# Performance work log

Measured on AMD Instinct MI355X. Metric: run time of the kernel, lower is better.

The kernel has to match this reference:

```python
import jax, jax.numpy as jnp
import numpy as np


def setup_inputs() -> dict:
    key = jax.random.key(0)
    k1, k2 = jax.random.split(key)
    pred = jax.random.normal(k1, (4, 8192, 3), dtype=jnp.float32)
    target = jax.random.normal(k2, (4, 8192, 3), dtype=jnp.float32)
    return {"pred": pred, "target": target}


def reference(pred, target):
    # Pairwise squared distances via the expansion ||p-q||^2 = ||p||^2 + ||q||^2 - 2 p.q
    # Avoids materializing the O(B*M*N*3) diff tensor of the naive broadcast.
    p_sq = jnp.sum(pred * pred, axis=-1)          # [B, M]
    q_sq = jnp.sum(target * target, axis=-1)      # [B, N]
    cross = jnp.einsum("bmd,bnd->bmn", pred, target)  # [B, M, N]
    dist_sq = p_sq[:, :, None] + q_sq[:, None, :] - 2.0 * cross  # [B, M, N]
    min_dist_pred = jnp.min(dist_sq, axis=2).mean(axis=1)    # [B] min over target per pred point
    min_dist_target = jnp.min(dist_sq, axis=1).mean(axis=1)  # [B] min over pred per target point
    return jnp.mean(min_dist_pred + min_dist_target)
```

## Files before the change

### kernel.cpp

```cpp
#include <hip/hip_runtime.h>


#define NBINS 256
#define XLO -6.0f
#define XHI 6.0f
#define TT 512
#define GP 64
#define TP 256
#define MAXTILES 34

#define THREADS 512
#define P 8
#define G 128
#define TILE 32
#define LSTRIDE (TILE + 1)
#define TSPLIT 2
#define BUFSZ (32 * LSTRIDE)

typedef float float2_t __attribute__((ext_vector_type(2)));
typedef float float4_t __attribute__((ext_vector_type(4)));

__global__ __launch_bounds__(THREADS) void bin_sort_kernel(
    const float* __restrict__ pred, const float* __restrict__ target,
    float4_t* __restrict__ sorted, int* __restrict__ binBase, int M) {
  int bs = blockIdx.x;
  int b = bs >> 1, side = bs & 1;
  const float* src = (side ? target : pred) + (size_t)b * M * 3;
  float4_t* out = sorted + (size_t)bs * M;
  int* bases = binBase + bs * (NBINS + 1);

  __shared__ int cnt[NBINS];
  __shared__ int scan[NBINS];
  __shared__ int cur[NBINS];
  int t = threadIdx.x;
  for (int i = t; i < NBINS; i += THREADS) cnt[i] = 0;
  __syncthreads();
  const float invW = (float)NBINS / (XHI - XLO);
  for (int i = t; i < M; i += THREADS) {
    float x = src[i * 3];
    int bin = (int)((x - XLO) * invW);
    bin = bin < 0 ? 0 : (bin > NBINS - 1 ? NBINS - 1 : bin);
    atomicAdd(&cnt[bin], 1);
  }
  __syncthreads();
  if (t < NBINS) scan[t] = cnt[t];
  __syncthreads();
  for (int off = 1; off < NBINS; off <<= 1) {
    int v = 0;
    if (t < NBINS && t >= off) v = scan[t - off];
    __syncthreads();
    if (t < NBINS) scan[t] += v;
    __syncthreads();
  }
  if (t < NBINS) {
    int excl = scan[t] - cnt[t];
    bases[t] = excl;
    cur[t] = excl;
  }
  if (t == 0) bases[NBINS] = M;
  __syncthreads();
  for (int i = t; i < M; i += THREADS) {
    float x = src[i * 3], y = src[i * 3 + 1], z = src[i * 3 + 2];
    int bin = (int)((x - XLO) * invW);
    bin = bin < 0 ? 0 : (bin > NBINS - 1 ? NBINS - 1 : bin);
    int pos = atomicAdd(&cur[bin], 1);
    out[pos] = (float4_t){x, y, z, x * x + y * y + z * z};
  }
}

__global__ __launch_bounds__(TP, 6) void chamfer_min_kernel(
    const float4_t* __restrict__ sorted, const int* __restrict__ binBase,
    float* __restrict__ wsmin, int M) {
  int bid = blockIdx.x;
  int pblk = bid & 127;
  int bd = bid >> 7;
  int dir = bd & 1, b = bd >> 1;
  int srcBS = b * 2 + dir;
  int refBS = b * 2 + (dir ^ 1);
  const float4_t* src = sorted + (size_t)srcBS * M;
  const float4_t* ref = sorted + (size_t)refBS * M;
  const int* rbase = binBase + refBS * (NBINS + 1);

  __shared__ float4_t tile[8 * 65];
  __shared__ float wred[TP / 64];

  int t = threadIdx.x;
  int c = t >> 3;
  int r = t & 7;
  int pbase = pblk * GP;

  float4_t v0 = src[pbase + c];
  float4_t v1 = src[pbase + c + 32];
  float ax0 = -2.f * v0.x, ay0 = -2.f * v0.y, az0 = -2.f * v0.z, cm0 = v0.w;
  float ax1 = -2.f * v1.x, ay1 = -2.f * v1.y, az1 = -2.f * v1.z, cm1 = v1.w;
  float mn0 = 3.0e38f, mn1 = 3.0e38f;

  const float W = (XHI - XLO) / (float)NBINS;
  float pxmn = src[pbase].x - W;
  float pxmx = src[pbase + GP - 1].x + W;

  int cl0 = (int)((pxmn - XLO) * (1.0f / W));
  cl0 = cl0 < 0 ? 0 : (cl0 > NBINS - 1 ? NBINS - 1 : cl0);
  int Lpos = rbase[cl0 + 1];
  int Rpos = Lpos;
  float bm = 3.0e38f;

  for (int iter = 0; iter < MAXTILES; ++iter) {
    float gapL = 3.0e38f, gapR = 3.0e38f;
    if (Lpos > 0) gapL = fmaxf(0.f, pxmn - (ref[Lpos - 1].x + W));
    if (Rpos < M) gapR = fmaxf(0.f, (ref[Rpos].x - W) - pxmx);
    bool leftDone = (Lpos <= 0) || (bm <= 0.999f * gapL * gapL);
    bool rightDone = (Rpos >= M) || (bm <= 0.999f * gapR * gapR);
    if (leftDone && rightDone) break;

    int availL = leftDone ? 0 : Lpos;
    int availR = rightDone ? 0 : (M - Rpos);
    int nL = availL < (TT / 2) ? availL : (TT / 2);
    int nR = availR < (TT - nL) ? availR : (TT - nL);
    nL = availL < (TT - nR) ? availL : (TT - nR);
    int lstart = Lpos - nL;
    int filled = nL + nR;
#pragma unroll
    for (int k = 0; k < TT / TP; ++k) {
      int i = t + TP * k;
      float4_t q = (float4_t){0.f, 0.f, 0.f, 3.0e38f};
      if (i < filled) {
        int idx = (i < nL) ? (lstart + i) : (Rpos + (i - nL));
        q = ref[idx];
      }
      tile[(i >> 6) * 65 + (i & 63)] = q;
    }
    Lpos = lstart;
    Rpos += nR;
    __syncthreads();

    const float4_t* tp = tile + r * 65;
#pragma unroll 2
    for (int j = 0; j < 64; j += 4) {
      float4_t q0 = tp[j + 0];
      float4_t q1 = tp[j + 1];
      float4_t q2 = tp[j + 2];
      float4_t q3 = tp[j + 3];
      float d00 = fmaf(ax0, q0.x, fmaf(ay0, q0.y, fmaf(az0, q0.z, q0.w)));
      float d01 = fmaf(ax0, q1.x, fmaf(ay0, q1.y, fmaf(az0, q1.z, q1.w)));
      float d02 = fmaf(ax0, q2.x, fmaf(ay0, q2.y, fmaf(az0, q2.z, q2.w)));
      float d03 = fmaf(ax0, q3.x, fmaf(ay0, q3.y, fmaf(az0, q3.z, q3.w)));
      mn0 = fminf(fminf(mn0, d00), d01);
      mn0 = fminf(fminf(mn0, d02), d03);
      float d10 = fmaf(ax1, q0.x, fmaf(ay1, q0.y, fmaf(az1, q0.z, q0.w)));
      float d11 = fmaf(ax1, q1.x, fmaf(ay1, q1.y, fmaf(az1, q1.z, q1.w)));
      float d12 = fmaf(ax1, q2.x, fmaf(ay1, q2.y, fmaf(az1, q2.z, q2.w)));
      float d13 = fmaf(ax1, q3.x, fmaf(ay1, q3.y, fmaf(az1, q3.z, q3.w)));
      mn1 = fminf(fminf(mn1, d10), d11);
      mn1 = fminf(fminf(mn1, d12), d13);
    }

    float f0 = mn0, f1 = mn1;
    f0 = fminf(f0, __shfl_xor(f0, 1, 64));
    f0 = fminf(f0, __shfl_xor(f0, 2, 64));
    f0 = fminf(f0, __shfl_xor(f0, 4, 64));
    f1 = fminf(f1, __shfl_xor(f1, 1, 64));
    f1 = fminf(f1, __shfl_xor(f1, 2, 64));
    f1 = fminf(f1, __shfl_xor(f1, 4, 64));
    float vv = fmaxf(f0 + cm0, f1 + cm1);
    vv = fmaxf(vv, __shfl_xor(vv, 8, 64));
    vv = fmaxf(vv, __shfl_xor(vv, 16, 64));
    vv = fmaxf(vv, __shfl_xor(vv, 32, 64));
    if ((t & 63) == 0) wred[t >> 6] = vv;
    __syncthreads();
    bm = fmaxf(fmaxf(wred[0], wred[1]), fmaxf(wred[2], wred[3]));
  }

  float f0 = mn0, f1 = mn1;
  f0 = fminf(f0, __shfl_xor(f0, 1, 64));
  f0 = fminf(f0, __shfl_xor(f0, 2, 64));
  f0 = fminf(f0, __shfl_xor(f0, 4, 64));
  f1 = fminf(f1, __shfl_xor(f1, 1, 64));
  f1 = fminf(f1, __shfl_xor(f1, 2, 64));
  f1 = fminf(f1, __shfl_xor(f1, 4, 64));
  if (r == 0) {
    wsmin[(size_t)srcBS * M + pbase + c] = f0 + cm0;
    wsmin[(size_t)srcBS * M + pbase + c + 32] = f1 + cm1;
  }
}

__global__ __launch_bounds__(256) void chamfer_reduce_kernel(
    const float* __restrict__ wsmin, float* __restrict__ out, int npts,
    float scale) {
  int tid = blockIdx.x * blockDim.x + threadIdx.x;
  int stride = gridDim.x * blockDim.x;
  double acc = 0.0;
  for (int p = tid; p < npts; p += stride) acc += (double)wsmin[p];
  for (int off = 32; off > 0; off >>= 1) acc += __shfl_down(acc, off, 64);
  __shared__ double wsum[256 / 64];
  int t = threadIdx.x;
  if ((t & 63) == 0) wsum[t >> 6] = acc;
  __syncthreads();
  if (t == 0) {
    double s = 0.0;
#pragma unroll
    for (int w = 0; w < 256 / 64; ++w) s += wsum[w];
    atomicAdd(out, (float)(s * (double)scale));
  }
}

__global__ __launch_bounds__(THREADS, 2) void chamfer_brute_kernel(
    const float* __restrict__ pred, const float* __restrict__ target,
    float* __restrict__ wsmin, int M) {
  const int blocksPerDir = M / G;
  int bid = blockIdx.x;
  int pblk = bid % blocksPerDir;
  int rest = bid / blocksPerDir;
  int ts = rest % TSPLIT;
  int bd = rest / TSPLIT;
  int dir = bd & 1;
  int b = bd >> 1;
  const float* src = (dir ? target : pred) + (size_t)b * M * 3;
  const float* ref = (dir ? pred : target) + (size_t)b * M * 3;

  __shared__ float4_t lds[2 * BUFSZ];

  int t = threadIdx.x;
  int g = t >> 4;
  int l = t & 15;

  float ax[P], ay[P], az[P];
  int pbase = pblk * G;
#pragma unroll
  for (int i = 0; i < P; ++i) {
    int p = pbase + l + 16 * i;
    float x = src[p * 3 + 0], y = src[p * 3 + 1], z = src[p * 3 + 2];
    ax[i] = -2.f * x;
    ay[i] = -2.f * y;
    az[i] = -2.f * z;
  }
  float mn[P];
#pragma unroll
  for (int i = 0; i < P; ++i) mn[i] = 3.0e38f;

  const int spanLen = M / TSPLIT;
  const int tbase = ts * spanLen;
  const int sliceLen = spanLen / 32;
  const int ntiles = sliceLen / TILE;

  const int sidx = 2 * t;
  const int ss = sidx >> 5;
  const int sjj = sidx & (TILE - 1);
  const int nb = tbase + ss * sliceLen + sjj;
  float rx0, ry0, rz0, rx1, ry1, rz1;

  {
    int n = nb;
    rx0 = ref[n * 3 + 0]; ry0 = ref[n * 3 + 1]; rz0 = ref[n * 3 + 2];
    rx1 = ref[n * 3 + 3]; ry1 = ref[n * 3 + 4]; rz1 = ref[n * 3 + 5];
    float4_t* dst = lds + ss * LSTRIDE + sjj;
    dst[0] = (float4_t){rx0, ry0, rz0, rx0 * rx0 + ry0 * ry0 + rz0 * rz0};
    dst[1] = (float4_t){rx1, ry1, rz1, rx1 * rx1 + ry1 * ry1 + rz1 * rz1};
  }
  __syncthreads();

  int cur = 0;
  for (int k = 0; k < ntiles; ++k) {
    if (k + 1 < ntiles) {
      int n = nb + (k + 1) * TILE;
      rx0 = ref[n * 3 + 0]; ry0 = ref[n * 3 + 1]; rz0 = ref[n * 3 + 2];
      rx1 = ref[n * 3 + 3]; ry1 = ref[n * 3 + 4]; rz1 = ref[n * 3 + 5];
    }
    const float4_t* tp = lds + cur * BUFSZ + g * LSTRIDE;
#pragma unroll 2
    for (int j = 0; j < TILE; j += 4) {
      float4_t q0 = tp[j + 0];
      float4_t q1 = tp[j + 1];
      float4_t q2 = tp[j + 2];
      float4_t q3 = tp[j + 3];
#pragma unroll
      for (int i = 0; i < P; ++i) {
        float d0 = fmaf(ax[i], q0.x, fmaf(ay[i], q0.y, fmaf(az[i], q0.z, q0.w)));
        float d1 = fmaf(ax[i], q1.x, fmaf(ay[i], q1.y, fmaf(az[i], q1.z, q1.w)));
        float d2 = fmaf(ax[i], q2.x, fmaf(ay[i], q2.y, fmaf(az[i], q2.z, q2.w)));
        float d3 = fmaf(ax[i], q3.x, fmaf(ay[i], q3.y, fmaf(az[i], q3.z, q3.w)));
        mn[i] = fminf(fminf(mn[i], d0), d1);
        mn[i] = fminf(fminf(mn[i], d2), d3);
      }
    }
    if (k + 1 < ntiles) {
      float4_t* dst = lds + (cur ^ 1) * BUFSZ + ss * LSTRIDE + sjj;
      dst[0] = (float4_t){rx0, ry0, rz0, rx0 * rx0 + ry0 * ry0 + rz0 * rz0};
      dst[1] = (float4_t){rx1, ry1, rz1, rx1 * rx1 + ry1 * ry1 + rz1 * rz1};
    }
    __syncthreads();
    cur ^= 1;
  }

  float* lmin = (float*)lds;
#pragma unroll
  for (int i = 0; i < P; ++i) lmin[g * G + (l + 16 * i)] = mn[i];
  __syncthreads();
  if (t < G) {
    float m = 3.0e38f;
#pragma unroll
    for (int s = 0; s < 32; ++s) m = fminf(m, lmin[s * G + t]);
    int p = pbase + t;
    float x = src[p * 3 + 0], y = src[p * 3 + 1], z = src[p * 3 + 2];
    int pid = (b * 2 + dir) * M + p;
    wsmin[(size_t)pid * TSPLIT + ts] = (x * x + y * y + z * z) + m;
  }
}

__global__ __launch_bounds__(256) void chamfer_reduce2_kernel(
    const float* __restrict__ wsmin, float* __restrict__ out, int npts,
    float scale) {
  int tid = blockIdx.x * blockDim.x + threadIdx.x;
  int stride = gridDim.x * blockDim.x;
  double acc = 0.0;
  for (int p = tid; p < npts; p += stride) {
    float2_t v = ((const float2_t*)wsmin)[p];
    acc += (double)fminf(v.x, v.y);
  }
  for (int off = 32; off > 0; off >>= 1) acc += __shfl_down(acc, off, 64);
  __shared__ double wsum[256 / 64];
  int t = threadIdx.x;
  if ((t & 63) == 0) wsum[t >> 6] = acc;
  __syncthreads();
  if (t == 0) {
    double s = 0.0;
#pragma unroll
    for (int w = 0; w < 256 / 64; ++w) s += wsum[w];
    atomicAdd(out, (float)(s * (double)scale));
  }
}

extern "C" void kernel_launch(void* const* d_in, const int* in_sizes, int n_in,
                              void* d_out, int out_size, void* d_ws,
                              size_t ws_size, hipStream_t stream) {
  const float* pred = (const float*)d_in[0];
  const float* target = (const float*)d_in[1];
  float* out = (float*)d_out;
  const int B = 4;
  const int M = in_sizes[0] / (B * 3);
  float scale = 1.0f / (float)(B * M);

  hipMemsetAsync(out, 0, sizeof(float), stream);

  size_t needWsmin = (size_t)B * 2 * M * 4;
  size_t needSorted = (size_t)B * 2 * M * 16;
  size_t needBins = (size_t)B * 2 * (NBINS + 1) * 4;
  size_t need = needWsmin + needSorted + needBins;

  if (ws_size >= need) {
    float* wsmin = (float*)d_ws;
    float4_t* sorted = (float4_t*)((char*)d_ws + needWsmin);
    int* binBase = (int*)((char*)sorted + needSorted);
    bin_sort_kernel<<<B * 2, THREADS, 0, stream>>>(pred, target, sorted,
                                                   binBase, M);
    int blocks = B * 2 * (M / GP);
    chamfer_min_kernel<<<blocks, TP, 0, stream>>>(sorted, binBase, wsmin, M);
    int npts = B * 2 * M;
    chamfer_reduce_kernel<<<64, 256, 0, stream>>>(wsmin, out, npts, scale);
  } else {
    float* wsmin = (float*)d_ws;
    int blocks = B * 2 * (M / G) * TSPLIT;
    chamfer_brute_kernel<<<blocks, THREADS, 0, stream>>>(pred, target, wsmin,
                                                         M);
    int npts = B * 2 * M;
    chamfer_reduce2_kernel<<<64, 256, 0, stream>>>(wsmin, out, npts, scale);
  }
}
```

Measured before the change: 113.4 us.

## Shrink chamfer search to single-wave blocks with double-buffered tile prefetch

The pruned nearest-neighbour kernel now runs one 64-thread wavefront per block handling 16 query points, which drops the cross-wave shared-memory max reduction and lets each block exit early on its own tighter bounding window. Reference tiles are double-buffered, so the next tile's global loads are issued into registers while the current tile is being computed. The bin-sort kernel also moves from 512 to 1024 threads. In exchange there are many more blocks, more tile iterations per block, and more repeated reference loads across blocks.

```diff
diff --git a/kernel.cpp b/kernel.cpp
--- a/kernel.cpp
+++ b/kernel.cpp
@@ -4,10 +4,16 @@
 #define NBINS 256
 #define XLO -6.0f
 #define XHI 6.0f
-#define TT 512
-#define GP 64
-#define TP 256
-#define MAXTILES 34
+
+#define TPW 64
+#define GPP 16
+#define TTT 256
+#define ROWS 8
+#define RLEN 32
+#define LROW 33
+#define MAXT 68
+
+#define BST 1024
 
 #define THREADS 512
 #define P 8
@@ -20,7 +26,7 @@
 typedef float float2_t __attribute__((ext_vector_type(2)));
 typedef float float4_t __attribute__((ext_vector_type(4)));
 
-__global__ __launch_bounds__(THREADS) void bin_sort_kernel(
+__global__ __launch_bounds__(BST) void bin_sort_kernel(
     const float* __restrict__ pred, const float* __restrict__ target,
     float4_t* __restrict__ sorted, int* __restrict__ binBase, int M) {
   int bs = blockIdx.x;
@@ -33,10 +39,10 @@
   __shared__ int scan[NBINS];
   __shared__ int cur[NBINS];
   int t = threadIdx.x;
-  for (int i = t; i < NBINS; i += THREADS) cnt[i] = 0;
+  for (int i = t; i < NBINS; i += BST) cnt[i] = 0;
   __syncthreads();
   const float invW = (float)NBINS / (XHI - XLO);
-  for (int i = t; i < M; i += THREADS) {
+  for (int i = t; i < M; i += BST) {
     float x = src[i * 3];
     int bin = (int)((x - XLO) * invW);
     bin = bin < 0 ? 0 : (bin > NBINS - 1 ? NBINS - 1 : bin);
@@ -59,7 +65,7 @@
   }
   if (t == 0) bases[NBINS] = M;
   __syncthreads();
-  for (int i = t; i < M; i += THREADS) {
+  for (int i = t; i < M; i += BST) {
     float x = src[i * 3], y = src[i * 3 + 1], z = src[i * 3 + 2];
     int bin = (int)((x - XLO) * invW);
     bin = bin < 0 ? 0 : (bin > NBINS - 1 ? NBINS - 1 : bin);
@@ -68,12 +74,13 @@
   }
 }
 
-__global__ __launch_bounds__(TP, 6) void chamfer_min_kernel(
+__global__ __launch_bounds__(TPW, 16) void chamfer_min_kernel(
     const float4_t* __restrict__ sorted, const int* __restrict__ binBase,
     float* __restrict__ wsmin, int M) {
+  const int bpd = M / GPP;
   int bid = blockIdx.x;
-  int pblk = bid & 127;
-  int bd = bid >> 7;
+  int pblk = bid % bpd;
+  int bd = bid / bpd;
   int dir = bd & 1, b = bd >> 1;
   int srcBS = b * 2 + dir;
   int refBS = b * 2 + (dir ^ 1);
@@ -81,62 +88,90 @@
   const float4_t* ref = sorted + (size_t)refBS * M;
   const int* rbase = binBase + refBS * (NBINS + 1);
 
-  __shared__ float4_t tile[8 * 65];
-  __shared__ float wred[TP / 64];
+  __shared__ float4_t tile[2][ROWS * LROW];
 
   int t = threadIdx.x;
   int c = t >> 3;
   int r = t & 7;
-  int pbase = pblk * GP;
+  int pbase = pblk * GPP;
 
   float4_t v0 = src[pbase + c];
-  float4_t v1 = src[pbase + c + 32];
+  float4_t v1 = src[pbase + c + 8];
   float ax0 = -2.f * v0.x, ay0 = -2.f * v0.y, az0 = -2.f * v0.z, cm0 = v0.w;
   float ax1 = -2.f * v1.x, ay1 = -2.f * v1.y, az1 = -2.f * v1.z, cm1 = v1.w;
   float mn0 = 3.0e38f, mn1 = 3.0e38f;
 
   const float W = (XHI - XLO) / (float)NBINS;
   float pxmn = src[pbase].x - W;
-  float pxmx = src[pbase + GP - 1].x + W;
-
-  int cl0 = (int)((pxmn - XLO) * (1.0f / W));
+  float pxmx = src[pbase + GPP - 1].x + W;
+
+  int cl0 = (int)((pxmn - XLO) * ((float)NBINS / (XHI - XLO)));
   cl0 = cl0 < 0 ? 0 : (cl0 > NBINS - 1 ? NBINS - 1 : cl0);
   int Lpos = rbase[cl0 + 1];
   int Rpos = Lpos;
-  float bm = 3.0e38f;
-
-  for (int iter = 0; iter < MAXTILES; ++iter) {
-    float gapL = 3.0e38f, gapR = 3.0e38f;
-    if (Lpos > 0) gapL = fmaxf(0.f, pxmn - (ref[Lpos - 1].x + W));
-    if (Rpos < M) gapR = fmaxf(0.f, (ref[Rpos].x - W) - pxmx);
-    bool leftDone = (Lpos <= 0) || (bm <= 0.999f * gapL * gapL);
-    bool rightDone = (Rpos >= M) || (bm <= 0.999f * gapR * gapR);
-    if (leftDone && rightDone) break;
-
-    int availL = leftDone ? 0 : Lpos;
-    int availR = rightDone ? 0 : (M - Rpos);
-    int nL = availL < (TT / 2) ? availL : (TT / 2);
-    int nR = availR < (TT - nL) ? availR : (TT - nL);
-    nL = availL < (TT - nR) ? availL : (TT - nR);
-    int lstart = Lpos - nL;
-    int filled = nL + nR;
-#pragma unroll
-    for (int k = 0; k < TT / TP; ++k) {
-      int i = t + TP * k;
-      float4_t q = (float4_t){0.f, 0.f, 0.f, 3.0e38f};
-      if (i < filled) {
-        int idx = (i < nL) ? (lstart + i) : (Rpos + (i - nL));
-        q = ref[idx];
-      }
-      tile[(i >> 6) * 65 + (i & 63)] = q;
-    }
+
+  float4_t st0, st1, st2, st3;
+  int nL, nR, lstart, fill;
+
+#define LDST(k_, reg_)                                              \
+  {                                                                 \
+    int i_ = t + TPW * (k_);                                        \
+    reg_ = (float4_t){0.f, 0.f, 0.f, 3.0e38f};                      \
+    if (i_ < fill) {                                                \
+      int idx_ = (i_ < nL) ? (lstart + i_) : (Rpos + (i_ - nL));    \
+      reg_ = ref[idx_];                                             \
+    }                                                               \
+  }
+#define WRST(k_, reg_, bb_)                                         \
+  {                                                                 \
+    int i_ = t + TPW * (k_);                                        \
+    tile[bb_][(i_ >> 5) * LROW + (i_ & 31)] = reg_;                 \
+  }
+
+  {
+    int aL = Lpos, aR = M - Rpos;
+    nL = aL < TTT / 2 ? aL : TTT / 2;
+    nR = aR < TTT - nL ? aR : TTT - nL;
+    nL = aL < TTT - nR ? aL : TTT - nR;
+    lstart = Lpos - nL;
+    fill = nL + nR;
+    LDST(0, st0) LDST(1, st1) LDST(2, st2) LDST(3, st3)
     Lpos = lstart;
     Rpos += nR;
-    __syncthreads();
-
-    const float4_t* tp = tile + r * 65;
-#pragma unroll 2
-    for (int j = 0; j < 64; j += 4) {
+    WRST(0, st0, 0) WRST(1, st1, 0) WRST(2, st2, 0) WRST(3, st3, 0)
+  }
+  float gxL = (Lpos > 0) ? ref[Lpos - 1].x : 0.f;
+  float gxR = (Rpos < M) ? ref[Rpos].x : 0.f;
+
+  float prevbm = 3.0e38f;
+  float f0 = 3.0e38f, f1 = 3.0e38f;
+  int cur = 0;
+  __syncthreads();
+
+  for (int it = 0; it < MAXT; ++it) {
+    int cL = Lpos, cR = Rpos;
+    float gapL = 3.0e38f, gapR = 3.0e38f;
+    if (cL > 0) gapL = fmaxf(0.f, pxmn - (gxL + W));
+    if (cR < M) gapR = fmaxf(0.f, (gxR - W) - pxmx);
+    bool exL = (cL <= 0), exR = (cR >= M);
+    bool dL = exL || (prevbm <= 0.999f * gapL * gapL);
+    bool dR = exR || (prevbm <= 0.999f * gapR * gapR);
+    if (!(dL && dR)) {
+      int aL = dL ? 0 : Lpos;
+      int aR = dR ? 0 : (M - Rpos);
+      nL = aL < TTT / 2 ? aL : TTT / 2;
+      nR = aR < TTT - nL ? aR : TTT - nL;
+      nL = aL < TTT - nR ? aL : TTT - nR;
+      lstart = Lpos - nL;
+      fill = nL + nR;
+      LDST(0, st0) LDST(1, st1) LDST(2, st2) LDST(3, st3)
+      Lpos = lstart;
+      Rpos += nR;
+    }
+
+    const float4_t* tp = &tile[cur][r * LROW];
+#pragma unroll
+    for (int j = 0; j < RLEN; j += 4) {
       float4_t q0 = tp[j + 0];
       float4_t q1 = tp[j + 1];
       float4_t q2 = tp[j + 2];
@@ -155,33 +190,38 @@
       mn1 = fminf(fminf(mn1, d12), d13);
     }
 
-    float f0 = mn0, f1 = mn1;
+    f0 = mn0;
     f0 = fminf(f0, __shfl_xor(f0, 1, 64));
     f0 = fminf(f0, __shfl_xor(f0, 2, 64));
     f0 = fminf(f0, __shfl_xor(f0, 4, 64));
+    f1 = mn1;
     f1 = fminf(f1, __shfl_xor(f1, 1, 64));
     f1 = fminf(f1, __shfl_xor(f1, 2, 64));
     f1 = fminf(f1, __shfl_xor(f1, 4, 64));
     float vv = fmaxf(f0 + cm0, f1 + cm1);
     vv = fmaxf(vv, __shfl_xor(vv, 8, 64));
     vv = fmaxf(vv, __shfl_xor(vv, 16, 64));
-    vv = fmaxf(vv, __shfl_xor(vv, 32, 64));
-    if ((t & 63) == 0) wred[t >> 6] = vv;
+    float bm = fmaxf(vv, __shfl_xor(vv, 32, 64));
+
+    bool fL = exL || (bm <= 0.999f * gapL * gapL);
+    bool fR = exR || (bm <= 0.999f * gapR * gapR);
+    if (fL && fR) break;
+    prevbm = bm;
+
+    WRST(0, st0, cur ^ 1) WRST(1, st1, cur ^ 1)
+    WRST(2, st2, cur ^ 1) WRST(3, st3, cur ^ 1)
+    gxL = (Lpos > 0) ? ref[Lpos - 1].x : 0.f;
+    gxR = (Rpos < M) ? ref[Rpos].x : 0.f;
+    cur ^= 1;
     __syncthreads();
-    bm = fmaxf(fmaxf(wred[0], wred[1]), fmaxf(wred[2], wred[3]));
-  }
-
-  float f0 = mn0, f1 = mn1;
-  f0 = fminf(f0, __shfl_xor(f0, 1, 64));
-  f0 = fminf(f0, __shfl_xor(f0, 2, 64));
-  f0 = fminf(f0, __shfl_xor(f0, 4, 64));
-  f1 = fminf(f1, __shfl_xor(f1, 1, 64));
-  f1 = fminf(f1, __shfl_xor(f1, 2, 64));
-  f1 = fminf(f1, __shfl_xor(f1, 4, 64));
+  }
+
   if (r == 0) {
     wsmin[(size_t)srcBS * M + pbase + c] = f0 + cm0;
-    wsmin[(size_t)srcBS * M + pbase + c + 32] = f1 + cm1;
-  }
+    wsmin[(size_t)srcBS * M + pbase + c + 8] = f1 + cm1;
+  }
+#undef LDST
+#undef WRST
 }
 
 __global__ __launch_bounds__(256) void chamfer_reduce_kernel(
@@ -351,10 +391,10 @@
     float* wsmin = (float*)d_ws;
     float4_t* sorted = (float4_t*)((char*)d_ws + needWsmin);
     int* binBase = (int*)((char*)sorted + needSorted);
-    bin_sort_kernel<<<B * 2, THREADS, 0, stream>>>(pred, target, sorted,
-                                                   binBase, M);
-    int blocks = B * 2 * (M / GP);
-    chamfer_min_kernel<<<blocks, TP, 0, stream>>>(sorted, binBase, wsmin, M);
+    bin_sort_kernel<<<B * 2, BST, 0, stream>>>(pred, target, sorted, binBase,
+                                               M);
+    int blocks = B * 2 * (M / GPP);
+    chamfer_min_kernel<<<blocks, TPW, 0, stream>>>(sorted, binBase, wsmin, M);
     int npts = B * 2 * M;
     chamfer_reduce_kernel<<<64, 256, 0, stream>>>(wsmin, out, npts, scale);
   } else {
```

Measured after the change: 114.4 us. Within noise of the previous version (+0.9%).

## Split chamfer search into bound pass and parallel fixed-size chunk blocks with atomicMin

Applied to the files above, without the earlier changes.

Replaces the per-slab serial tile-expansion loop, which synchronized and recomputed a block-wide bound after every tile, with a two-stage scheme. A bound kernel first computes an upper bound from a small local window around each point, then derives the reference range for the slab. A chunk kernel then launches one block per 512-point chunk of that range, and blocks past the needed count exit early. Per-point minima are merged with atomicMin on float bits, with the workspace pre-filled by a memset. The sort kernel also moves to 1024 threads. This adds launches, a memset and global atomics, and relies on distances being non-negative for the unsigned comparison.

```diff
diff --git a/kernel.cpp b/kernel.cpp
--- a/kernel.cpp
+++ b/kernel.cpp
@@ -4,10 +4,13 @@
 #define NBINS 256
 #define XLO -6.0f
 #define XHI 6.0f
-#define TT 512
-#define GP 64
-#define TP 256
-#define MAXTILES 34
+
+#define SLABP 64
+#define CHUNK 512
+#define MAXCH 16
+#define UBN 64
+
+#define BST 1024
 
 #define THREADS 512
 #define P 8
@@ -20,7 +23,7 @@
 typedef float float2_t __attribute__((ext_vector_type(2)));
 typedef float float4_t __attribute__((ext_vector_type(4)));
 
-__global__ __launch_bounds__(THREADS) void bin_sort_kernel(
+__global__ __launch_bounds__(BST) void bin_sort_kernel(
     const float* __restrict__ pred, const float* __restrict__ target,
     float4_t* __restrict__ sorted, int* __restrict__ binBase, int M) {
   int bs = blockIdx.x;
@@ -33,10 +36,10 @@
   __shared__ int scan[NBINS];
   __shared__ int cur[NBINS];
   int t = threadIdx.x;
-  for (int i = t; i < NBINS; i += THREADS) cnt[i] = 0;
+  for (int i = t; i < NBINS; i += BST) cnt[i] = 0;
   __syncthreads();
   const float invW = (float)NBINS / (XHI - XLO);
-  for (int i = t; i < M; i += THREADS) {
+  for (int i = t; i < M; i += BST) {
     float x = src[i * 3];
     int bin = (int)((x - XLO) * invW);
     bin = bin < 0 ? 0 : (bin > NBINS - 1 ? NBINS - 1 : bin);
@@ -59,7 +62,7 @@
   }
   if (t == 0) bases[NBINS] = M;
   __syncthreads();
-  for (int i = t; i < M; i += THREADS) {
+  for (int i = t; i < M; i += BST) {
     float x = src[i * 3], y = src[i * 3 + 1], z = src[i * 3 + 2];
     int bin = (int)((x - XLO) * invW);
     bin = bin < 0 ? 0 : (bin > NBINS - 1 ? NBINS - 1 : bin);
@@ -68,119 +71,130 @@
   }
 }
 
-__global__ __launch_bounds__(TP, 6) void chamfer_min_kernel(
+__global__ __launch_bounds__(SLABP) void bound_kernel(
     const float4_t* __restrict__ sorted, const int* __restrict__ binBase,
-    float* __restrict__ wsmin, int M) {
+    int* __restrict__ hdr, int M) {
+  int s = blockIdx.x;
+  int spd = M / SLABP;
+  int bs = s / spd;
+  int pblk = s % spd;
+  const float4_t* src = sorted + (size_t)bs * M;
+  const float4_t* ref = sorted + (size_t)(bs ^ 1) * M;
+  const int* rbase = binBase + (bs ^ 1) * (NBINS + 1);
+
+  int t = threadIdx.x;
+  int pbase = pblk * SLABP;
+  float4_t p = src[pbase + t];
+  float ax = -2.f * p.x, ay = -2.f * p.y, az = -2.f * p.z;
+
+  const float W = (XHI - XLO) / (float)NBINS;
+  const float invW = 1.0f / W;
+  int bin = (int)((p.x - XLO) * invW);
+  bin = bin < 0 ? 0 : (bin > NBINS - 1 ? NBINS - 1 : bin);
+  int pos0 = rbase[bin];
+  int lo = pos0 - UBN; lo = lo < 0 ? 0 : lo;
+  int hi = pos0 + UBN; hi = hi > M ? M : hi;
+  float ub = 3.0e38f;
+  for (int j = lo; j < hi; ++j) {
+    float4_t q = ref[j];
+    float d = fmaf(ax, q.x, fmaf(ay, q.y, fmaf(az, q.z, q.w)));
+    ub = fminf(ub, d);
+  }
+  ub += p.w;
+
+  float bmax = ub, xmn = p.x, xmx = p.x;
+#pragma unroll
+  for (int off = 1; off < 64; off <<= 1) {
+    bmax = fmaxf(bmax, __shfl_xor(bmax, off, 64));
+    xmn = fminf(xmn, __shfl_xor(xmn, off, 64));
+    xmx = fmaxf(xmx, __shfl_xor(xmx, off, 64));
+  }
+  if (t == 0) {
+    float r = sqrtf(bmax);
+    int lb = (int)floorf((xmn - r - XLO) * invW) - 1;
+    lb = lb < 0 ? 0 : (lb > NBINS - 1 ? NBINS - 1 : lb);
+    int rb = (int)floorf((xmx + r - XLO) * invW) + 1;
+    rb = rb < 0 ? 0 : (rb > NBINS - 1 ? NBINS - 1 : rb);
+    int Lpos = rbase[lb];
+    int Rpos = rbase[rb + 1];
+    int nch = (Rpos - Lpos + CHUNK - 1) / CHUNK;
+    hdr[s * 4 + 0] = Lpos;
+    hdr[s * 4 + 1] = Rpos;
+    hdr[s * 4 + 2] = nch;
+    hdr[s * 4 + 3] = 0;
+  }
+}
+
+__global__ __launch_bounds__(256, 8) void chunk_kernel(
+    const float4_t* __restrict__ sorted, const int* __restrict__ hdr,
+    unsigned int* __restrict__ wsmin, int M) {
   int bid = blockIdx.x;
-  int pblk = bid & 127;
-  int bd = bid >> 7;
-  int dir = bd & 1, b = bd >> 1;
-  int srcBS = b * 2 + dir;
-  int refBS = b * 2 + (dir ^ 1);
-  const float4_t* src = sorted + (size_t)srcBS * M;
-  const float4_t* ref = sorted + (size_t)refBS * M;
-  const int* rbase = binBase + refBS * (NBINS + 1);
+  int s = bid >> 4;
+  int ci = bid & 15;
+  int nch = hdr[s * 4 + 2];
+  if (ci >= nch) return;
+  int Lpos = hdr[s * 4 + 0];
+  int Rpos = hdr[s * 4 + 1];
+  int spd = M / SLABP;
+  int bs = s / spd;
+  int pblk = s % spd;
+  const float4_t* src = sorted + (size_t)bs * M;
+  const float4_t* ref = sorted + (size_t)(bs ^ 1) * M;
+  int pbase = pblk * SLABP;
+  int start = Lpos + ci * CHUNK;
+  int fill = Rpos - start;
+  fill = fill > CHUNK ? CHUNK : fill;
 
   __shared__ float4_t tile[8 * 65];
-  __shared__ float wred[TP / 64];
-
-  int t = threadIdx.x;
+  int t = threadIdx.x;
+#pragma unroll
+  for (int k = 0; k < 2; ++k) {
+    int i = t + 256 * k;
+    float4_t q = (float4_t){0.f, 0.f, 0.f, 3.0e38f};
+    if (i < fill) q = ref[start + i];
+    tile[(i >> 6) * 65 + (i & 63)] = q;
+  }
+  __syncthreads();
+
   int c = t >> 3;
   int r = t & 7;
-  int pbase = pblk * GP;
-
   float4_t v0 = src[pbase + c];
   float4_t v1 = src[pbase + c + 32];
   float ax0 = -2.f * v0.x, ay0 = -2.f * v0.y, az0 = -2.f * v0.z, cm0 = v0.w;
   float ax1 = -2.f * v1.x, ay1 = -2.f * v1.y, az1 = -2.f * v1.z, cm1 = v1.w;
   float mn0 = 3.0e38f, mn1 = 3.0e38f;
 
-  const float W = (XHI - XLO) / (float)NBINS;
-  float pxmn = src[pbase].x - W;
-  float pxmx = src[pbase + GP - 1].x + W;
-
-  int cl0 = (int)((pxmn - XLO) * (1.0f / W));
-  cl0 = cl0 < 0 ? 0 : (cl0 > NBINS - 1 ? NBINS - 1 : cl0);
-  int Lpos = rbase[cl0 + 1];
-  int Rpos = Lpos;
-  float bm = 3.0e38f;
-
-  for (int iter = 0; iter < MAXTILES; ++iter) {
-    float gapL = 3.0e38f, gapR = 3.0e38f;
-    if (Lpos > 0) gapL = fmaxf(0.f, pxmn - (ref[Lpos - 1].x + W));
-    if (Rpos < M) gapR = fmaxf(0.f, (ref[Rpos].x - W) - pxmx);
-    bool leftDone = (Lpos <= 0) || (bm <= 0.999f * gapL * gapL);
-    bool rightDone = (Rpos >= M) || (bm <= 0.999f * gapR * gapR);
-    if (leftDone && rightDone) break;
-
-    int availL = leftDone ? 0 : Lpos;
-    int availR = rightDone ? 0 : (M - Rpos);
-    int nL = availL < (TT / 2) ? availL : (TT / 2);
-    int nR = availR < (TT - nL) ? availR : (TT - nL);
-    nL = availL < (TT - nR) ? availL : (TT - nR);
-    int lstart = Lpos - nL;
-    int filled = nL + nR;
-#pragma unroll
-    for (int k = 0; k < TT / TP; ++k) {
-      int i = t + TP * k;
-      float4_t q = (float4_t){0.f, 0.f, 0.f, 3.0e38f};
-      if (i < filled) {
-        int idx = (i < nL) ? (lstart + i) : (Rpos + (i - nL));
-        q = ref[idx];
-      }
-      tile[(i >> 6) * 65 + (i & 63)] = q;
-    }
-    Lpos = lstart;
-    Rpos += nR;
-    __syncthreads();
-
-    const float4_t* tp = tile + r * 65;
+  const float4_t* tp = tile + r * 65;
 #pragma unroll 2
-    for (int j = 0; j < 64; j += 4) {
-      float4_t q0 = tp[j + 0];
-      float4_t q1 = tp[j + 1];
-      float4_t q2 = tp[j + 2];
-      float4_t q3 = tp[j + 3];
-      float d00 = fmaf(ax0, q0.x, fmaf(ay0, q0.y, fmaf(az0, q0.z, q0.w)));
-      float d01 = fmaf(ax0, q1.x, fmaf(ay0, q1.y, fmaf(az0, q1.z, q1.w)));
-      float d02 = fmaf(ax0, q2.x, fmaf(ay0, q2.y, fmaf(az0, q2.z, q2.w)));
-      float d03 = fmaf(ax0, q3.x, fmaf(ay0, q3.y, fmaf(az0, q3.z, q3.w)));
-      mn0 = fminf(fminf(mn0, d00), d01);
-      mn0 = fminf(fminf(mn0, d02), d03);
-      float d10 = fmaf(ax1, q0.x, fmaf(ay1, q0.y, fmaf(az1, q0.z, q0.w)));
-      float d11 = fmaf(ax1, q1.x, fmaf(ay1, q1.y, fmaf(az1, q1.z, q1.w)));
-      float d12 = fmaf(ax1, q2.x, fmaf(ay1, q2.y, fmaf(az1, q2.z, q2.w)));
-      float d13 = fmaf(ax1, q3.x, fmaf(ay1, q3.y, fmaf(az1, q3.z, q3.w)));
-      mn1 = fminf(fminf(mn1, d10), d11);
-      mn1 = fminf(fminf(mn1, d12), d13);
-    }
-
-    float f0 = mn0, f1 = mn1;
-    f0 = fminf(f0, __shfl_xor(f0, 1, 64));
-    f0 = fminf(f0, __shfl_xor(f0, 2, 64));
-    f0 = fminf(f0, __shfl_xor(f0, 4, 64));
-    f1 = fminf(f1, __shfl_xor(f1, 1, 64));
-    f1 = fminf(f1, __shfl_xor(f1, 2, 64));
-    f1 = fminf(f1, __shfl_xor(f1, 4, 64));
-    float vv = fmaxf(f0 + cm0, f1 + cm1);
-    vv = fmaxf(vv, __shfl_xor(vv, 8, 64));
-    vv = fmaxf(vv, __shfl_xor(vv, 16, 64));
-    vv = fmaxf(vv, __shfl_xor(vv, 32, 64));
-    if ((t & 63) == 0) wred[t >> 6] = vv;
-    __syncthreads();
-    bm = fmaxf(fmaxf(wred[0], wred[1]), fmaxf(wred[2], wred[3]));
-  }
-
-  float f0 = mn0, f1 = mn1;
-  f0 = fminf(f0, __shfl_xor(f0, 1, 64));
-  f0 = fminf(f0, __shfl_xor(f0, 2, 64));
-  f0 = fminf(f0, __shfl_xor(f0, 4, 64));
-  f1 = fminf(f1, __shfl_xor(f1, 1, 64));
-  f1 = fminf(f1, __shfl_xor(f1, 2, 64));
-  f1 = fminf(f1, __shfl_xor(f1, 4, 64));
+  for (int j = 0; j < 64; j += 4) {
+    float4_t q0 = tp[j + 0];
+    float4_t q1 = tp[j + 1];
+    float4_t q2 = tp[j + 2];
+    float4_t q3 = tp[j + 3];
+    float d00 = fmaf(ax0, q0.x, fmaf(ay0, q0.y, fmaf(az0, q0.z, q0.w)));
+    float d01 = fmaf(ax0, q1.x, fmaf(ay0, q1.y, fmaf(az0, q1.z, q1.w)));
+    float d02 = fmaf(ax0, q2.x, fmaf(ay0, q2.y, fmaf(az0, q2.z, q2.w)));
+    float d03 = fmaf(ax0, q3.x, fmaf(ay0, q3.y, fmaf(az0, q3.z, q3.w)));
+    mn0 = fminf(fminf(mn0, d00), d01);
+    mn0 = fminf(fminf(mn0, d02), d03);
+    float d10 = fmaf(ax1, q0.x, fmaf(ay1, q0.y, fmaf(az1, q0.z, q0.w)));
+    float d11 = fmaf(ax1, q1.x, fmaf(ay1, q1.y, fmaf(az1, q1.z, q1.w)));
+    float d12 = fmaf(ax1, q2.x, fmaf(ay1, q2.y, fmaf(az1, q2.z, q2.w)));
+    float d13 = fmaf(ax1, q3.x, fmaf(ay1, q3.y, fmaf(az1, q3.z, q3.w)));
+    mn1 = fminf(fminf(mn1, d10), d11);
+    mn1 = fminf(fminf(mn1, d12), d13);
+  }
+
+  mn0 = fminf(mn0, __shfl_xor(mn0, 1, 64));
+  mn0 = fminf(mn0, __shfl_xor(mn0, 2, 64));
+  mn0 = fminf(mn0, __shfl_xor(mn0, 4, 64));
+  mn1 = fminf(mn1, __shfl_xor(mn1, 1, 64));
+  mn1 = fminf(mn1, __shfl_xor(mn1, 2, 64));
+  mn1 = fminf(mn1, __shfl_xor(mn1, 4, 64));
   if (r == 0) {
-    wsmin[(size_t)srcBS * M + pbase + c] = f0 + cm0;
-    wsmin[(size_t)srcBS * M + pbase + c + 32] = f1 + cm1;
+    size_t base = (size_t)bs * M + pbase;
+    atomicMin(&wsmin[base + c], __float_as_uint(mn0 + cm0));
+    atomicMin(&wsmin[base + c + 32], __float_as_uint(mn1 + cm1));
   }
 }
 
@@ -345,16 +359,23 @@
   size_t needWsmin = (size_t)B * 2 * M * 4;
   size_t needSorted = (size_t)B * 2 * M * 16;
   size_t needBins = (size_t)B * 2 * (NBINS + 1) * 4;
-  size_t need = needWsmin + needSorted + needBins;
+  int nslabs = B * 2 * (M / SLABP);
+  size_t needHdr = (size_t)nslabs * 4 * 4;
+  size_t need = needWsmin + needSorted + needBins + needHdr;
 
   if (ws_size >= need) {
     float* wsmin = (float*)d_ws;
     float4_t* sorted = (float4_t*)((char*)d_ws + needWsmin);
     int* binBase = (int*)((char*)sorted + needSorted);
-    bin_sort_kernel<<<B * 2, THREADS, 0, stream>>>(pred, target, sorted,
-                                                   binBase, M);
-    int blocks = B * 2 * (M / GP);
-    chamfer_min_kernel<<<blocks, TP, 0, stream>>>(sorted, binBase, wsmin, M);
+    int* hdr = (int*)((char*)binBase + needBins);
+
+    hipMemsetAsync(wsmin, 0x7F, needWsmin, stream);
+
+    bin_sort_kernel<<<B * 2, BST, 0, stream>>>(pred, target, sorted, binBase,
+                                               M);
+    bound_kernel<<<nslabs, SLABP, 0, stream>>>(sorted, binBase, hdr, M);
+    chunk_kernel<<<nslabs * MAXCH, 256, 0, stream>>>(
+        sorted, hdr, (unsigned int*)wsmin, M);
     int npts = B * 2 * M;
     chamfer_reduce_kernel<<<64, 256, 0, stream>>>(wsmin, out, npts, scale);
   } else {
```

After: 138.2 us. +21.9%, slower.
